# Kernel optimization log

Measured on AMD Instinct MI355X. Metric: run time of the kernel, lower is better.

Reference implementation:

```python
import jax, jax.numpy as jnp
import numpy as np

A = 32          # num input capsule types
PSIZE = 16      # caps_size (pose matrix 4x4)
MD = 4          # mat_dim = sqrt(caps_size)
NCLS = 10       # output capsules / classes
KF = 5          # routing kernel (final_shape)
KK = KF * KF
KKA = KK * A
ITERS = 3
FINAL_LAMBDA = 0.01
EPS = 1e-12
LN2PI = float(np.log(2.0 * np.pi))
BN_EPS = 1e-5


def unfold(x, k, stride, pad):
    # torch.nn.functional.unfold: [b,C,h,w] -> [b, C*k*k, L], (c, kh, kw) channel-major
    b, c, h, w = x.shape
    if pad:
        x = jnp.pad(x, ((0, 0), (0, 0), (pad, pad), (pad, pad)))
    oh = (h + 2 * pad - k) // stride + 1
    ow = (w + 2 * pad - k) // stride + 1
    cols = jnp.stack([
        jnp.stack([x[:, :, i:i + stride * oh:stride, j:j + stride * ow:stride]
                   for j in range(k)], axis=3)
        for i in range(k)], axis=2)          # [b, c, k, k, oh, ow]
    return cols.reshape(b, c * k * k, oh * ow)


def conv3x3(x, w):
    return jax.lax.conv_general_dilated(x, w, (1, 1), [(1, 1), (1, 1)],
                                        dimension_numbers=('NCHW', 'OIHW', 'NCHW'))


def bn_inf(x, g, b, m, v):
    scale = g / jnp.sqrt(v + BN_EPS)
    return (x - m[None, :, None, None]) * scale[None, :, None, None] + b[None, :, None, None]


def em_routing(a_in, pose, W, beta_u, beta_a):
    b = a_in.shape[0]
    # pose votes
    pu = unfold(pose, KF, 1, 0)                     # [b, A*PSIZE*KK, l]
    l = pu.shape[-1]
    pu = pu.reshape(b, A, PSIZE, KK, l).transpose(0, 4, 3, 1, 2).reshape(b, l, KKA, PSIZE)
    pm = pu.reshape(b, l, KKA, MD, MD)[:, :, :, None]        # [b,l,kkA,1,md,md]
    v = jnp.matmul(pm, W)                                    # [b,l,kkA,B,md,md]
    v = v.reshape(b, l, KKA, NCLS, PSIZE)
    # activations
    au = unfold(a_in, KF, 1, 0).reshape(b, A, KK, l).transpose(0, 3, 2, 1).reshape(b, l, KKA)
    r = jnp.ones((b, l, KKA, NCLS, 1), v.dtype)
    a_out = mu = None
    for i in range(ITERS):
        lam = FINAL_LAMBDA * (1.0 - 0.95 ** (i + 1))
        # M-step
        rw = r * au[:, :, :, None, None]
        r_sum = rw.sum(axis=2, keepdims=True)                # [b,l,1,B,1]
        coeff = rw / (r_sum + EPS)
        mu = (coeff * v).sum(axis=2, keepdims=True)          # [b,l,1,B,psize]
        sigma_sq = (coeff * (v - mu) ** 2).sum(axis=2, keepdims=True) + EPS
        r_s = r_sum[:, :, 0]                                 # [b,l,B,1]
        sig = sigma_sq[:, :, 0]                              # [b,l,B,psize]
        cost_h = (beta_u + 0.5 * jnp.log(sig)) * r_s         # log(sqrt(s)) = 0.5*log(s)
        a_out = jax.nn.sigmoid(lam * (beta_a - cost_h.sum(axis=3)))   # [b,l,B]
        if i < ITERS - 1:
            # E-step (note: log(sigma_sq * ln2pi) as in original code)
            ln_p = (-0.5 * jnp.sum(jnp.log(sigma_sq * LN2PI), axis=-1)
                    - jnp.sum((v - mu) ** 2 / (2.0 * sigma_sq), axis=-1))   # [b,l,kkA,B]
            ln_ap = ln_p + jnp.log(a_out)[:, :, None, :]
            r = jax.nn.softmax(ln_ap, axis=-1)[..., None]
    oh = int(np.floor(np.sqrt(l)))
    pose_out = mu[:, :, 0].reshape(b, l, -1).transpose(0, 2, 1).reshape(b, -1, oh, oh)
    a_map = a_out.transpose(0, 2, 1).reshape(b, -1, oh, oh)
    return a_map, pose_out


def setup_inputs():
    key = jax.random.key(0)
    ks = jax.random.split(key, 14)
    batch = 256
    x = jax.random.normal(ks[0], (batch, 512, 5, 5), jnp.float32)
    w_a = jax.random.normal(ks[1], (A, 512, 3, 3), jnp.float32) * 0.02
    w_pose = jax.random.normal(ks[2], (A * PSIZE, 512, 3, 3), jnp.float32) * 0.02
    bn_a_g = 1.0 + 0.1 * jax.random.normal(ks[3], (A,), jnp.float32)
    bn_a_b = 0.1 * jax.random.normal(ks[4], (A,), jnp.float32)
    bn_a_m = 0.1 * jax.random.normal(ks[5], (A,), jnp.float32)
    bn_a_v = jax.random.uniform(ks[6], (A,), jnp.float32, 0.5, 1.5)
    C2 = A * PSIZE
    bn_p_g = 1.0 + 0.1 * jax.random.normal(ks[7], (C2,), jnp.float32)
    bn_p_b = 0.1 * jax.random.normal(ks[8], (C2,), jnp.float32)
    bn_p_m = 0.1 * jax.random.normal(ks[9], (C2,), jnp.float32)
    bn_p_v = jax.random.uniform(ks[10], (C2,), jnp.float32, 0.5, 1.5)
    W = jax.random.normal(ks[11], (KKA, NCLS, MD, MD), jnp.float32) * 0.25
    beta_u = jnp.zeros((1, 1, NCLS, 1), jnp.float32)
    beta_a = jnp.zeros((1, 1, NCLS), jnp.float32)
    return {"x": x, "w_a": w_a, "w_pose": w_pose,
            "bn_a_g": bn_a_g, "bn_a_b": bn_a_b, "bn_a_m": bn_a_m, "bn_a_v": bn_a_v,
            "bn_p_g": bn_p_g, "bn_p_b": bn_p_b, "bn_p_m": bn_p_m, "bn_p_v": bn_p_v,
            "W": W, "beta_u": beta_u, "beta_a": beta_a}


def reference(x, w_a, w_pose, bn_a_g, bn_a_b, bn_a_m, bn_a_v,
              bn_p_g, bn_p_b, bn_p_m, bn_p_v, W, beta_u, beta_a):
    a = jax.nn.sigmoid(bn_inf(conv3x3(x, w_a), bn_a_g, bn_a_b, bn_a_m, bn_a_v))
    pose = bn_inf(conv3x3(x, w_pose), bn_p_g, bn_p_b, bn_p_m, bn_p_v)
    a_map, _ = em_routing(a, pose, W, beta_u, beta_a)
    out = a_map.reshape(a_map.shape[0], -1)          # [b, 10]
    out = out / out.sum(axis=1, keepdims=True)
    return jnp.log(out)
```

## Files before the change

### kernel.cpp

```cpp
#include <hip/hip_runtime.h>
#include <math.h>

#define CIN 512
#define NCLS 10
#define KDIM 4608
#define NTOT 6400
#define MPAD 640
#define BK 128
#define NKT 36
#define NABLK (5 * NKT)
#define LN2PI_F 1.8378770664093453f

typedef __attribute__((ext_vector_type(8))) short bf16x8;
typedef __attribute__((ext_vector_type(4))) float f32x4;

typedef const __attribute__((address_space(1))) void* gas_ptr;
typedef __attribute__((address_space(3))) void* las_ptr;

__device__ __forceinline__ void async_copy16(const void* g, void* l) {
    __builtin_amdgcn_global_load_lds((gas_ptr)g, (las_ptr)l, 16, 0, 0);
}

__device__ __forceinline__ unsigned short f2bf(float f) {
    unsigned int u = __float_as_uint(f);
    u = (u + 0x7fffu + ((u >> 16) & 1u)) >> 16;
    return (unsigned short)u;
}
__device__ __forceinline__ float fexp(float x) { return __expf(x); }
__device__ __forceinline__ float flog(float x) { return __logf(x); }

__global__ __launch_bounds__(256) void pack_a_kernel(
    const float* __restrict__ w_pose, const float* __restrict__ w_a,
    const float* __restrict__ bn_p_g, const float* __restrict__ bn_p_b,
    const float* __restrict__ bn_p_m, const float* __restrict__ bn_p_v,
    const float* __restrict__ bn_a_g, const float* __restrict__ bn_a_b,
    const float* __restrict__ bn_a_m, const float* __restrict__ bn_a_v,
    const float* __restrict__ Wm,
    unsigned short* __restrict__ At, unsigned short* __restrict__ Wmb,
    float* __restrict__ sc, float* __restrict__ bi)
{
    const int blk = blockIdx.x;
    const int t = threadIdx.x;

    if (blk >= NABLK) {
        const int chunk = (blk - NABLK) * 256 + t;
        if (chunk < 16000) {
            const float4* s4 = reinterpret_cast<const float4*>(Wm + (size_t)chunk * 8);
            float4 x0 = s4[0], x1 = s4[1];
            int4 o;
            o.x = (int)f2bf(x0.x) | ((int)f2bf(x0.y) << 16);
            o.y = (int)f2bf(x0.z) | ((int)f2bf(x0.w) << 16);
            o.z = (int)f2bf(x1.x) | ((int)f2bf(x1.y) << 16);
            o.w = (int)f2bf(x1.z) | ((int)f2bf(x1.w) << 16);
            reinterpret_cast<int4*>(Wmb + (size_t)chunk * 8)[0] = o;
        }
        return;
    }

    const int mblk = blk / NKT;
    if (blk == 0) {
        for (int i = t; i < MPAD; i += 256) {
            float s = 0.f, b = 0.f;
            if (i < 512) {
                s = bn_p_g[i] / sqrtf(bn_p_v[i] + 1e-5f);
                b = bn_p_b[i] - bn_p_m[i] * s;
            } else if (i < 544) {
                const int j = i - 512;
                s = bn_a_g[j] / sqrtf(bn_a_v[j] + 1e-5f);
                b = bn_a_b[j] - bn_a_m[j] * s;
            }
            sc[i] = s; bi[i] = b;
        }
    }

    const int kt = blk - mblk * NKT;
    #pragma unroll
    for (int j = 0; j < 8; ++j) {
        const int c = t + j * 256;
        const int kc8 = c >> 7, slot = c & 127;
        const int row = mblk * 128 + (slot ^ (kc8 << 2));
        const int k0 = (kt * 16 + kc8) * 8;
        float v[8] = {0.f,0.f,0.f,0.f,0.f,0.f,0.f,0.f};
        if (row < 512) {
            const float4* s4 = reinterpret_cast<const float4*>(w_pose + (size_t)row * KDIM + k0);
            float4 x0 = s4[0], x1 = s4[1];
            v[0]=x0.x; v[1]=x0.y; v[2]=x0.z; v[3]=x0.w;
            v[4]=x1.x; v[5]=x1.y; v[6]=x1.z; v[7]=x1.w;
        } else if (row < 544) {
            const float4* s4 = reinterpret_cast<const float4*>(w_a + (size_t)(row - 512) * KDIM + k0);
            float4 x0 = s4[0], x1 = s4[1];
            v[0]=x0.x; v[1]=x0.y; v[2]=x0.z; v[3]=x0.w;
            v[4]=x1.x; v[5]=x1.y; v[6]=x1.z; v[7]=x1.w;
        }
        int4 o;
        o.x = (int)f2bf(v[0]) | ((int)f2bf(v[1]) << 16);
        o.y = (int)f2bf(v[2]) | ((int)f2bf(v[3]) << 16);
        o.z = (int)f2bf(v[4]) | ((int)f2bf(v[5]) << 16);
        o.w = (int)f2bf(v[6]) | ((int)f2bf(v[7]) << 16);
        reinterpret_cast<int4*>(At + ((((size_t)blk) << 11) + c) * 8)[0] = o;
    }
}

__global__ __launch_bounds__(1024) void pack_b_kernel(
    const float* __restrict__ x, unsigned short* __restrict__ Bt)
{
    __shared__ __align__(16) float xs[CIN * 25];
    const int b = blockIdx.x;
    const int t = threadIdx.x;
    const float4* xb = reinterpret_cast<const float4*>(x + (size_t)b * (CIN * 25));
    for (int f4 = t; f4 < (CIN * 25) / 4; f4 += 1024)
        reinterpret_cast<float4*>(xs)[f4] = xb[f4];
    __syncthreads();

    for (int w = t; w < 25 * (KDIM / 8); w += 1024) {
        const int px = w / (KDIM / 8);
        const int ch = w - px * (KDIM / 8);
        const int py = px / 5, qx = px % 5;
        const int k0 = ch * 8;
        unsigned short v[8];
        #pragma unroll
        for (int j = 0; j < 8; ++j) {
            const int k = k0 + j;
            const int ci = k / 9;
            const int kk = k - ci * 9;
            const int dy = kk / 3, dx = kk - dy * 3;
            const int yy = py + dy - 1, xx = qx + dx - 1;
            const bool ok = (yy >= 0) & (yy < 5) & (xx >= 0) & (xx < 5);
            v[j] = ok ? f2bf(xs[ci * 25 + yy * 5 + xx]) : (unsigned short)0;
        }
        int4 o;
        o.x = (int)v[0] | ((int)v[1] << 16);
        o.y = (int)v[2] | ((int)v[3] << 16);
        o.z = (int)v[4] | ((int)v[5] << 16);
        o.w = (int)v[6] | ((int)v[7] << 16);
        const int n = b * 25 + px;
        const int nblk = n >> 7, nr = n & 127;
        const int kt = k0 >> 7;
        const int kc8 = (k0 >> 3) & 15;
        const int c = kc8 * 128 + (nr ^ (kc8 << 2));
        reinterpret_cast<int4*>(Bt + ((((size_t)(nblk * NKT + kt)) << 11) + c) * 8)[0] = o;
    }
}

__global__ __launch_bounds__(512) void gemm_kernel(
    const unsigned short* __restrict__ At,
    const unsigned short* __restrict__ Bt,
    const float* __restrict__ sc, const float* __restrict__ bi,
    float* __restrict__ C)
{
    __shared__ __align__(16) unsigned char smem[131072];
    const int t = threadIdx.x;
    const int mblk = blockIdx.x, nblk = blockIdx.y;
    const int m0 = mblk * 128, n0 = nblk * 128;
    const int lane = t & 63, w = t >> 6;
    const int g = w >> 2, wq = w & 3;
    const int wm = wq >> 1, wn = wq & 1;
    const int row16 = lane & 15, quad = lane >> 4;

    f32x4 acc[4][4] = {};

    const unsigned short* gAbase = At + (((size_t)mblk * NKT) << 14);
    const unsigned short* gBbase = Bt + (((size_t)nblk * NKT) << 14);

    #define STAGE(kt, s)                                                      \
    {                                                                         \
        unsigned short* As_ = (unsigned short*)(smem + (s) * 65536);          \
        unsigned short* Bs_ = As_ + 16384;                                    \
        const unsigned short* ga = gAbase + ((size_t)(kt) << 14);             \
        const unsigned short* gb = gBbase + ((size_t)(kt) << 14);             \
        _Pragma("unroll")                                                     \
        for (int j = 0; j < 4; ++j) {                                         \
            async_copy16(ga + ((size_t)(j * 512 + t) << 3),                   \
                         As_ + ((size_t)(j * 512 + w * 64) << 3));            \
            async_copy16(gb + ((size_t)(j * 512 + t) << 3),                   \
                         Bs_ + ((size_t)(j * 512 + w * 64) << 3));            \
        }                                                                     \
    }

    #define COMPUTE(s)                                                        \
    {                                                                         \
        const unsigned short* As_ = (const unsigned short*)(smem + (s) * 65536);\
        const unsigned short* Bs_ = As_ + 16384;                              \
        _Pragma("unroll")                                                     \
        for (int ks = 0; ks < 2; ++ks) {                                      \
            const int kc8b = g * 8 + ks * 4 + quad;                           \
            const int sw = kc8b << 2;                                         \
            bf16x8 af[4], bfr[4];                                             \
            _Pragma("unroll")                                                 \
            for (int mt = 0; mt < 4; ++mt)                                    \
                af[mt] = *reinterpret_cast<const bf16x8*>(                    \
                    &As_[(size_t)(kc8b * 128 + ((wm * 64 + mt * 16 + row16) ^ sw)) * 8]);\
            _Pragma("unroll")                                                 \
            for (int nt = 0; nt < 4; ++nt)                                    \
                bfr[nt] = *reinterpret_cast<const bf16x8*>(                   \
                    &Bs_[(size_t)(kc8b * 128 + ((wn * 64 + nt * 16 + row16) ^ sw)) * 8]);\
            _Pragma("unroll")                                                 \
            for (int mt = 0; mt < 4; ++mt)                                    \
                _Pragma("unroll")                                             \
                for (int nt = 0; nt < 4; ++nt)                                \
                    acc[mt][nt] = __builtin_amdgcn_mfma_f32_16x16x32_bf16(    \
                        af[mt], bfr[nt], acc[mt][nt], 0, 0, 0);               \
        }                                                                     \
    }

    STAGE(0, 0);
    for (int kt = 0; kt < NKT; ++kt) {
        __syncthreads();
        if (kt + 1 < NKT) STAGE(kt + 1, (kt + 1) & 1);
        COMPUTE(kt & 1);
    }
    #undef STAGE
    #undef COMPUTE

    float* mb = (float*)smem;
    #pragma unroll
    for (int rnd = 0; rnd < 2; ++rnd) {
        __syncthreads();
        if (g == 1 && (wq >> 1) == rnd) {
            f32x4* dst = (f32x4*)(mb + (wq & 1) * 4096);
            #pragma unroll
            for (int i = 0; i < 16; ++i)
                dst[i * 64 + lane] = acc[i >> 2][i & 3];
        }
        __syncthreads();
        if (g == 0 && (wq >> 1) == rnd) {
            const f32x4* src = (const f32x4*)(mb + (wq & 1) * 4096);
            #pragma unroll
            for (int i = 0; i < 16; ++i)
                acc[i >> 2][i & 3] += src[i * 64 + lane];
        }
    }

    if (g == 0) {
        #pragma unroll
        for (int mt = 0; mt < 4; ++mt) {
            const int mbase = m0 + wm * 64 + mt * 16 + quad * 4;
            if (mbase >= 544) continue;
            #pragma unroll
            for (int rg = 0; rg < 4; ++rg) {
                const int m = mbase + rg;
                const float s = sc[m], bbx = bi[m];
                const bool is_a = (m >= 512);
                #pragma unroll
                for (int nt = 0; nt < 4; ++nt) {
                    const int n = n0 + wn * 64 + nt * 16 + row16;
                    float v = fmaf(acc[mt][nt][rg], s, bbx);
                    if (is_a) v = 1.f / (1.f + fexp(-v));
                    C[(size_t)m * NTOT + n] = v;
                }
            }
        }
    }
}

__device__ __forceinline__ void loadW_bf(const unsigned short* wp, float* wv) {
    const int4* q = reinterpret_cast<const int4*>(wp);
    const int4 q0 = q[0], q1 = q[1];
    const unsigned int u[8] = {(unsigned)q0.x,(unsigned)q0.y,(unsigned)q0.z,(unsigned)q0.w,
                               (unsigned)q1.x,(unsigned)q1.y,(unsigned)q1.z,(unsigned)q1.w};
    #pragma unroll
    for (int i = 0; i < 8; ++i) {
        wv[2*i]   = __uint_as_float(u[i] << 16);
        wv[2*i+1] = __uint_as_float(u[i] & 0xFFFF0000u);
    }
}

__device__ __forceinline__ void vote16(const float* pmp, const float* wv, float* vv) {
    float pm[16];
    const float4* pr = reinterpret_cast<const float4*>(pmp);
    float4 p0 = pr[0], p1 = pr[1], p2 = pr[2], p3 = pr[3];
    pm[0]=p0.x; pm[1]=p0.y; pm[2]=p0.z; pm[3]=p0.w;
    pm[4]=p1.x; pm[5]=p1.y; pm[6]=p1.z; pm[7]=p1.w;
    pm[8]=p2.x; pm[9]=p2.y; pm[10]=p2.z; pm[11]=p2.w;
    pm[12]=p3.x; pm[13]=p3.y; pm[14]=p3.z; pm[15]=p3.w;
    #pragma unroll
    for (int r = 0; r < 4; ++r)
        #pragma unroll
        for (int s = 0; s < 4; ++s) {
            float av = 0.f;
            #pragma unroll
            for (int tt = 0; tt < 4; ++tt)
                av = fmaf(pm[r*4+tt], wv[tt*4+s], av);
            vv[r*4+s] = av;
        }
}

__global__ __launch_bounds__(640, 2) void em_kernel(
    const float* __restrict__ C,
    const unsigned short* __restrict__ Wmb,
    const float* __restrict__ beta_u, const float* __restrict__ beta_a,
    float* __restrict__ out)
{
    __shared__ __align__(16) float psh[25][32][20];
    __shared__ float aush[800];
    __shared__ float lnq[NCLS][800];
    __shared__ float redsh[NCLS][34];
    __shared__ float mu_sh[NCLS][16];
    __shared__ float i2s_sh[NCLS][16];
    __shared__ float Kc_sh[NCLS];
    __shared__ float aout_sh[NCLS];

    const int b = blockIdx.x, t = threadIdx.x;
    const int h = t >= 320 ? 1 : 0;
    const int th = t - h * 320;
    const int c = th >> 5, a = th & 31;
    const int kkA = h ? 13 : 0, kkB = h ? 25 : 13;

    const float* pb = C + (size_t)b * 25;
    for (int f = t; f < 12800; f += 640) {
        const int c2 = f / 25, px = f - c2 * 25;
        psh[px][c2 >> 4][c2 & 15] = pb[(size_t)c2 * NTOT + px];
    }
    const float* ab = C + (size_t)512 * NTOT + (size_t)b * 25;
    for (int f = t; f < 800; f += 640) {
        const int ci = f / 25, px = f - ci * 25;
        aush[px * 32 + ci] = ab[(size_t)ci * NTOT + px];
    }
    __syncthreads();

    const float bu = beta_u[c], ba = beta_a[c];
    const float lam_tab[3] = {0.01f * (1.f - 0.95f),
                              0.01f * (1.f - 0.95f * 0.95f),
                              0.01f * (1.f - 0.95f * 0.95f * 0.95f)};
    float muL[16], i2sL[16], KcL = 0.f;
    float S0, S1[16], S2[16];

    const unsigned short* wbase = Wmb + ((size_t)a * NCLS + c) * 16;

    for (int it = 0; it < 3; ++it) {
        if (it > 0) {
            for (int kk = kkA; kk < kkB; ++kk) {
                float wv[16], vv[16];
                loadW_bf(wbase + (size_t)kk * 5120, wv);
                vote16(&psh[kk][a][0], wv, vv);
                float q = KcL;
                #pragma unroll
                for (int p = 0; p < 16; ++p) {
                    const float d = vv[p] - muL[p];
                    q -= d * d * i2sL[p];
                }
                lnq[c][kk * 32 + a] = q;
            }
            __syncthreads();
        }

        S0 = 0.f;
        #pragma unroll
        for (int p = 0; p < 16; ++p) { S1[p] = 0.f; S2[p] = 0.f; }

        for (int kk = kkA; kk < kkB; ++kk) {
            float wv[16], vv[16];
            loadW_bf(wbase + (size_t)kk * 5120, wv);
            vote16(&psh[kk][a][0], wv, vv);
            const int m = kk * 32 + a;
            float rw;
            if (it == 0) {
                rw = aush[m];
            } else {
                float qv[NCLS];
                #pragma unroll
                for (int cc = 0; cc < NCLS; ++cc) qv[cc] = lnq[cc][m];
                float mx = qv[0];
                #pragma unroll
                for (int cc = 1; cc < NCLS; ++cc) mx = fmaxf(mx, qv[cc]);
                float den = 0.f;
                #pragma unroll
                for (int cc = 0; cc < NCLS; ++cc) den += fexp(qv[cc] - mx);
                const float r = fexp(qv[c] - mx) * __builtin_amdgcn_rcpf(den);
                rw = r * aush[m];
            }
            S0 += rw;
            #pragma unroll
            for (int p = 0; p < 16; ++p) {
                const float rv = rw * vv[p];
                S1[p] += rv;
                S2[p] = fmaf(rv, vv[p], S2[p]);
            }
        }

        #pragma unroll
        for (int off = 16; off >= 1; off >>= 1) {
            S0 += __shfl_xor(S0, off);
            #pragma unroll
            for (int p = 0; p < 16; ++p) {
                S1[p] += __shfl_xor(S1[p], off);
                S2[p] += __shfl_xor(S2[p], off);
            }
        }

        if (h == 1 && a == 0) {
            redsh[c][0] = S0;
            #pragma unroll
            for (int p = 0; p < 16; ++p) { redsh[c][1 + p] = S1[p]; redsh[c][17 + p] = S2[p]; }
        }
        __syncthreads();
        if (h == 0 && a == 0) {
            S0 += redsh[c][0];
            #pragma unroll
            for (int p = 0; p < 16; ++p) { S1[p] += redsh[c][1 + p]; S2[p] += redsh[c][17 + p]; }

            const float lam = lam_tab[it];
            const float s0e = S0 + 1e-12f;
            const float inv = 1.f / s0e;
            float costsum = 0.f, slg = 0.f;
            float mu_[16], sg_[16];
            #pragma unroll
            for (int p = 0; p < 16; ++p) {
                mu_[p] = S1[p] * inv;
                const float sg = (S2[p] - 2.f * mu_[p] * S1[p] + mu_[p] * mu_[p] * S0) * inv
                                 + 1e-12f;
                sg_[p] = sg;
                costsum += bu + 0.5f * flog(sg);
            }
            costsum *= S0;
            const float aout = 1.f / (1.f + fexp(-(lam * (ba - costsum))));
            aout_sh[c] = aout;
            if (it < 2) {
                #pragma unroll
                for (int p = 0; p < 16; ++p) {
                    mu_sh[c][p] = mu_[p];
                    i2s_sh[c][p] = 0.5f / sg_[p];
                    slg += flog(sg_[p] * LN2PI_F);
                }
                Kc_sh[c] = flog(aout) - 0.5f * slg;
            }
        }
        __syncthreads();
        if (it < 2) {
            #pragma unroll
            for (int p = 0; p < 16; ++p) { muL[p] = mu_sh[c][p]; i2sL[p] = i2s_sh[c][p]; }
            KcL = Kc_sh[c];
        }
    }

    if (t < NCLS) {
        float s = 0.f;
        #pragma unroll
        for (int cc = 0; cc < NCLS; ++cc) s += aout_sh[cc];
        out[b * NCLS + t] = flog(aout_sh[t] / s);
    }
}

extern "C" void kernel_launch(void* const* d_in, const int* in_sizes, int n_in,
                              void* d_out, int out_size, void* d_ws, size_t ws_size,
                              hipStream_t stream) {
    const float* x      = (const float*)d_in[0];
    const float* w_a    = (const float*)d_in[1];
    const float* w_pose = (const float*)d_in[2];
    const float* bn_a_g = (const float*)d_in[3];
    const float* bn_a_b = (const float*)d_in[4];
    const float* bn_a_m = (const float*)d_in[5];
    const float* bn_a_v = (const float*)d_in[6];
    const float* bn_p_g = (const float*)d_in[7];
    const float* bn_p_b = (const float*)d_in[8];
    const float* bn_p_m = (const float*)d_in[9];
    const float* bn_p_v = (const float*)d_in[10];
    const float* Wm     = (const float*)d_in[11];
    const float* beta_u = (const float*)d_in[12];
    const float* beta_a = (const float*)d_in[13];
    float* out = (float*)d_out;

    char* p = (char*)d_ws;
    unsigned short* At  = (unsigned short*)p;  p += (size_t)MPAD * KDIM * 2;
    unsigned short* Bt  = (unsigned short*)p;  p += (size_t)NTOT * KDIM * 2;
    unsigned short* Wmb = (unsigned short*)p;  p += (size_t)800 * NCLS * 16 * 2;
    float* C  = (float*)p;                     p += (size_t)544 * NTOT * 4;
    float* sc = (float*)p;                     p += MPAD * 4;
    float* bi = (float*)p;                     p += MPAD * 4;

    pack_a_kernel<<<NABLK + 63, 256, 0, stream>>>(w_pose, w_a,
                                                  bn_p_g, bn_p_b, bn_p_m, bn_p_v,
                                                  bn_a_g, bn_a_b, bn_a_m, bn_a_v,
                                                  Wm, At, Wmb, sc, bi);
    pack_b_kernel<<<256, 1024, 0, stream>>>(x, Bt);
    dim3 gg(MPAD / 128, NTOT / 128);
    gemm_kernel<<<gg, 512, 0, stream>>>(At, Bt, sc, bi, C);
    em_kernel<<<256, 640, 0, stream>>>(C, Wmb, beta_u, beta_a, out);
}
```

Baseline: 270.3 us.

## Split EM routing work across pose-element halves instead of kernel-position halves

The two thread halves of each block now each handle 8 of the 16 pose elements over all 25 kernel positions, instead of splitting kernel positions and holding all 16 elements. This halves the per-thread accumulator registers. The E-step log-likelihoods become two partial arrays that are summed in shared memory. The softmax routing weights are precomputed once into shared memory instead of being recomputed inside the M-step loop. In exchange each thread reloads the full W row for every position, the kernel adds extra barriers, and it doubles the shared lnq buffer. Launch bounds drop from 2 blocks to 1 block per CU, which may reduce occupancy given the larger shared memory.

```diff
diff --git a/kernel.cpp b/kernel.cpp
--- a/kernel.cpp
+++ b/kernel.cpp
@@ -265,27 +265,7 @@
     }
 }
 
-__device__ __forceinline__ void vote16(const float* pmp, const float* wv, float* vv) {
-    float pm[16];
-    const float4* pr = reinterpret_cast<const float4*>(pmp);
-    float4 p0 = pr[0], p1 = pr[1], p2 = pr[2], p3 = pr[3];
-    pm[0]=p0.x; pm[1]=p0.y; pm[2]=p0.z; pm[3]=p0.w;
-    pm[4]=p1.x; pm[5]=p1.y; pm[6]=p1.z; pm[7]=p1.w;
-    pm[8]=p2.x; pm[9]=p2.y; pm[10]=p2.z; pm[11]=p2.w;
-    pm[12]=p3.x; pm[13]=p3.y; pm[14]=p3.z; pm[15]=p3.w;
-    #pragma unroll
-    for (int r = 0; r < 4; ++r)
-        #pragma unroll
-        for (int s = 0; s < 4; ++s) {
-            float av = 0.f;
-            #pragma unroll
-            for (int tt = 0; tt < 4; ++tt)
-                av = fmaf(pm[r*4+tt], wv[tt*4+s], av);
-            vv[r*4+s] = av;
-        }
-}
-
-__global__ __launch_bounds__(640, 2) void em_kernel(
+__global__ __launch_bounds__(640, 1) void em_kernel(
     const float* __restrict__ C,
     const unsigned short* __restrict__ Wmb,
     const float* __restrict__ beta_u, const float* __restrict__ beta_a,
@@ -293,18 +273,19 @@
 {
     __shared__ __align__(16) float psh[25][32][20];
     __shared__ float aush[800];
-    __shared__ float lnq[NCLS][800];
-    __shared__ float redsh[NCLS][34];
+    __shared__ float lnqp[2][NCLS][800];
     __shared__ float mu_sh[NCLS][16];
     __shared__ float i2s_sh[NCLS][16];
+    __shared__ float costp[2][NCLS];
+    __shared__ float slgp[2][NCLS];
     __shared__ float Kc_sh[NCLS];
     __shared__ float aout_sh[NCLS];
 
     const int b = blockIdx.x, t = threadIdx.x;
-    const int h = t >= 320 ? 1 : 0;
-    const int th = t - h * 320;
+    const int rh = (t >= 320) ? 1 : 0;
+    const int th = t - rh * 320;
     const int c = th >> 5, a = th & 31;
-    const int kkA = h ? 13 : 0, kkB = h ? 25 : 13;
+    float* rwsh = &lnqp[1][0][0];
 
     const float* pb = C + (size_t)b * 25;
     for (int f = t; f < 12800; f += 640) {
@@ -319,62 +300,89 @@
     __syncthreads();
 
     const float bu = beta_u[c], ba = beta_a[c];
-    const float lam_tab[3] = {0.01f * (1.f - 0.95f),
-                              0.01f * (1.f - 0.95f * 0.95f),
-                              0.01f * (1.f - 0.95f * 0.95f * 0.95f)};
-    float muL[16], i2sL[16], KcL = 0.f;
-    float S0, S1[16], S2[16];
-
+    float muL[8], i2sL[8], KcL = 0.f;
     const unsigned short* wbase = Wmb + ((size_t)a * NCLS + c) * 16;
 
+    #define VOTE_HALF(kk, vv)                                                \
+        float pm[8], wv[16];                                                 \
+        {                                                                    \
+            const float4* pr = reinterpret_cast<const float4*>(&psh[kk][a][rh * 8]); \
+            const float4 p0 = pr[0], p1 = pr[1];                             \
+            pm[0]=p0.x; pm[1]=p0.y; pm[2]=p0.z; pm[3]=p0.w;                  \
+            pm[4]=p1.x; pm[5]=p1.y; pm[6]=p1.z; pm[7]=p1.w;                  \
+            loadW_bf(wbase + (size_t)(kk) * 5120, wv);                       \
+            _Pragma("unroll")                                                \
+            for (int jr = 0; jr < 2; ++jr) {                                 \
+                _Pragma("unroll")                                            \
+                for (int s = 0; s < 4; ++s) {                                \
+                    float av = 0.f;                                          \
+                    _Pragma("unroll")                                        \
+                    for (int tt = 0; tt < 4; ++tt)                           \
+                        av = fmaf(pm[jr*4+tt], wv[tt*4+s], av);              \
+                    vv[jr*4+s] = av;                                         \
+                }                                                            \
+            }                                                                \
+        }
+
+    float p95 = 1.f;
     for (int it = 0; it < 3; ++it) {
+        p95 *= 0.95f;
+        const float lam = 0.01f * (1.f - p95);
+
         if (it > 0) {
-            for (int kk = kkA; kk < kkB; ++kk) {
-                float wv[16], vv[16];
-                loadW_bf(wbase + (size_t)kk * 5120, wv);
-                vote16(&psh[kk][a][0], wv, vv);
-                float q = KcL;
+            for (int kk = 0; kk < 25; ++kk) {
+                float vv[8];
+                VOTE_HALF(kk, vv);
+                float q = (rh == 0) ? KcL : 0.f;
                 #pragma unroll
-                for (int p = 0; p < 16; ++p) {
-                    const float d = vv[p] - muL[p];
-                    q -= d * d * i2sL[p];
+                for (int j = 0; j < 8; ++j) {
+                    const float d = vv[j] - muL[j];
+                    q -= d * d * i2sL[j];
                 }
-                lnq[c][kk * 32 + a] = q;
+                lnqp[rh][c][kk * 32 + a] = q;
             }
             __syncthreads();
-        }
-
-        S0 = 0.f;
+            {
+                float* l0 = &lnqp[0][0][0];
+                const float* l1 = &lnqp[1][0][0];
+                for (int f = t; f < 8000; f += 640) l0[f] += l1[f];
+            }
+            __syncthreads();
+            {
+                const int k0 = rh ? 13 : 0, k1 = rh ? 25 : 13;
+                for (int kk = k0; kk < k1; ++kk) {
+                    const int m = kk * 32 + a;
+                    float qv[NCLS];
+                    #pragma unroll
+                    for (int cc = 0; cc < NCLS; ++cc) qv[cc] = lnqp[0][cc][m];
+                    float mx = qv[0];
+                    #pragma unroll
+                    for (int cc = 1; cc < NCLS; ++cc) mx = fmaxf(mx, qv[cc]);
+                    float den = 0.f;
+                    #pragma unroll
+                    for (int cc = 0; cc < NCLS; ++cc) den += fexp(qv[cc] - mx);
+                    rwsh[c * 800 + m] = fexp(qv[c] - mx) * __builtin_amdgcn_rcpf(den)
+                                        * aush[m];
+                }
+            }
+            __syncthreads();
+        }
+
+        float S0 = 0.f, S1[8], S2[8];
         #pragma unroll
-        for (int p = 0; p < 16; ++p) { S1[p] = 0.f; S2[p] = 0.f; }
-
-        for (int kk = kkA; kk < kkB; ++kk) {
-            float wv[16], vv[16];
-            loadW_bf(wbase + (size_t)kk * 5120, wv);
-            vote16(&psh[kk][a][0], wv, vv);
+        for (int j = 0; j < 8; ++j) { S1[j] = 0.f; S2[j] = 0.f; }
+
+        for (int kk = 0; kk < 25; ++kk) {
+            float vv[8];
+            VOTE_HALF(kk, vv);
             const int m = kk * 32 + a;
-            float rw;
-            if (it == 0) {
-                rw = aush[m];
-            } else {
-                float qv[NCLS];
-                #pragma unroll
-                for (int cc = 0; cc < NCLS; ++cc) qv[cc] = lnq[cc][m];
-                float mx = qv[0];
-                #pragma unroll
-                for (int cc = 1; cc < NCLS; ++cc) mx = fmaxf(mx, qv[cc]);
-                float den = 0.f;
-                #pragma unroll
-                for (int cc = 0; cc < NCLS; ++cc) den += fexp(qv[cc] - mx);
-                const float r = fexp(qv[c] - mx) * __builtin_amdgcn_rcpf(den);
-                rw = r * aush[m];
-            }
+            const float rw = (it == 0) ? aush[m] : rwsh[c * 800 + m];
             S0 += rw;
             #pragma unroll
-            for (int p = 0; p < 16; ++p) {
-                const float rv = rw * vv[p];
-                S1[p] += rv;
-                S2[p] = fmaf(rv, vv[p], S2[p]);
+            for (int j = 0; j < 8; ++j) {
+                const float rv = rw * vv[j];
+                S1[j] += rv;
+                S2[j] = fmaf(rv, vv[j], S2[j]);
             }
         }
 
@@ -382,53 +390,43 @@
         for (int off = 16; off >= 1; off >>= 1) {
             S0 += __shfl_xor(S0, off);
             #pragma unroll
-            for (int p = 0; p < 16; ++p) {
-                S1[p] += __shfl_xor(S1[p], off);
-                S2[p] += __shfl_xor(S2[p], off);
-            }
-        }
-
-        if (h == 1 && a == 0) {
-            redsh[c][0] = S0;
-            #pragma unroll
-            for (int p = 0; p < 16; ++p) { redsh[c][1 + p] = S1[p]; redsh[c][17 + p] = S2[p]; }
-        }
-        __syncthreads();
-        if (h == 0 && a == 0) {
-            S0 += redsh[c][0];
-            #pragma unroll
-            for (int p = 0; p < 16; ++p) { S1[p] += redsh[c][1 + p]; S2[p] += redsh[c][17 + p]; }
-
-            const float lam = lam_tab[it];
+            for (int j = 0; j < 8; ++j) {
+                S1[j] += __shfl_xor(S1[j], off);
+                S2[j] += __shfl_xor(S2[j], off);
+            }
+        }
+
+        if (a == 0) {
             const float s0e = S0 + 1e-12f;
             const float inv = 1.f / s0e;
-            float costsum = 0.f, slg = 0.f;
-            float mu_[16], sg_[16];
-            #pragma unroll
-            for (int p = 0; p < 16; ++p) {
-                mu_[p] = S1[p] * inv;
-                const float sg = (S2[p] - 2.f * mu_[p] * S1[p] + mu_[p] * mu_[p] * S0) * inv
+            float cost_ = 0.f, slg_ = 0.f;
+            #pragma unroll
+            for (int j = 0; j < 8; ++j) {
+                const float mu_ = S1[j] * inv;
+                const float sg = (S2[j] - 2.f * mu_ * S1[j] + mu_ * mu_ * S0) * inv
                                  + 1e-12f;
-                sg_[p] = sg;
-                costsum += bu + 0.5f * flog(sg);
-            }
-            costsum *= S0;
+                cost_ += bu + 0.5f * flog(sg);
+                slg_ += flog(sg * LN2PI_F);
+                mu_sh[c][rh * 8 + j] = mu_;
+                i2s_sh[c][rh * 8 + j] = 0.5f / sg;
+            }
+            costp[rh][c] = cost_;
+            slgp[rh][c] = slg_;
+        }
+        __syncthreads();
+        if (a == 0 && rh == 0) {
+            const float costsum = (costp[0][c] + costp[1][c]) * S0;
             const float aout = 1.f / (1.f + fexp(-(lam * (ba - costsum))));
             aout_sh[c] = aout;
-            if (it < 2) {
-                #pragma unroll
-                for (int p = 0; p < 16; ++p) {
-                    mu_sh[c][p] = mu_[p];
-                    i2s_sh[c][p] = 0.5f / sg_[p];
-                    slg += flog(sg_[p] * LN2PI_F);
-                }
-                Kc_sh[c] = flog(aout) - 0.5f * slg;
-            }
+            Kc_sh[c] = flog(aout) - 0.5f * (slgp[0][c] + slgp[1][c]);
         }
         __syncthreads();
         if (it < 2) {
             #pragma unroll
-            for (int p = 0; p < 16; ++p) { muL[p] = mu_sh[c][p]; i2sL[p] = i2s_sh[c][p]; }
+            for (int j = 0; j < 8; ++j) {
+                muL[j] = mu_sh[c][rh * 8 + j];
+                i2sL[j] = i2s_sh[c][rh * 8 + j];
+            }
             KcL = Kc_sh[c];
         }
     }
@@ -439,6 +437,7 @@
         for (int cc = 0; cc < NCLS; ++cc) s += aout_sh[cc];
         out[b * NCLS + t] = flog(aout_sh[t] / s);
     }
+    #undef VOTE_HALF
 }
 
 extern "C" void kernel_launch(void* const* d_in, const int* in_sizes, int n_in,
```

Measured after the change: 264.6 us. -2.1%, faster.
